# Kernel optimization log

Hardware: AMD Instinct MI355X
Metric: run time of the kernel (lower is better)

The kernel has to match this reference:

```python
import jax, jax.numpy as jnp
import numpy as np

N = 100000
E = 1600000
NUM_GRAPHS = 128
IN_C = 11
HID = 128


def setup_inputs() -> dict:
    key = jax.random.key(0)
    ks = jax.random.split(key, 16)
    x = jax.random.normal(ks[0], (N, IN_C), dtype=jnp.float32)
    edge_index = jax.random.randint(ks[1], (2, E), 0, N, dtype=jnp.int64)
    batch = jnp.sort(jax.random.randint(ks[2], (N,), 0, NUM_GRAPHS, dtype=jnp.int64))
    s_in = 1.0 / np.sqrt(IN_C)
    s_h = 1.0 / np.sqrt(HID)
    params = {
        'W1': jax.random.normal(ks[3], (IN_C, HID), jnp.float32) * s_in,
        'b1': jnp.zeros((HID,), jnp.float32),
        'W2': jax.random.normal(ks[4], (HID, HID), jnp.float32) * s_h,
        'b2': jnp.zeros((HID,), jnp.float32),
        'W4': jax.random.normal(ks[5], (HID, HID), jnp.float32) * s_h,
        'b4': jnp.zeros((HID,), jnp.float32),
        'Wd1': jax.random.normal(ks[6], (HID, HID), jnp.float32) * s_h,
        'bd1': jnp.zeros((HID,), jnp.float32),
        'Wd2': jax.random.normal(ks[7], (HID, HID), jnp.float32) * s_h,
        'bd2': jnp.zeros((HID,), jnp.float32),
        'Wo': jax.random.normal(ks[8], (HID, 1), jnp.float32) * s_h,
        'bo': jnp.zeros((1,), jnp.float32),
    }
    return {'x': x, 'edge_index': edge_index, 'batch': batch, **params}


def _gcn_norm(edge_index, n_nodes):
    # add self loops, compute symmetric normalization (PyG GCNConv defaults)
    loop = jnp.arange(n_nodes, dtype=edge_index.dtype)
    row = jnp.concatenate([edge_index[0], loop])
    col = jnp.concatenate([edge_index[1], loop])
    deg = jax.ops.segment_sum(jnp.ones_like(col, dtype=jnp.float32), col,
                              num_segments=n_nodes)
    dinv = jnp.where(deg > 0, jax.lax.rsqrt(deg), 0.0)
    norm = dinv[row] * dinv[col]  # [E+N]
    return row, col, norm


def _gcn_conv(h, row, col, norm, W, b, n_nodes):
    h = h @ W  # dense lin first (PyG order)
    msg = norm[:, None] * h[row]            # gather + normalize
    out = jax.ops.segment_sum(msg, col, num_segments=n_nodes)  # scatter-add
    return out + b


def reference(x, edge_index, batch, W1, b1, W2, b2, W4, b4,
              Wd1, bd1, Wd2, bd2, Wo, bo):
    n = x.shape[0]
    row, col, norm = _gcn_norm(edge_index, n)
    # dropout is identity in eval mode
    h = jax.nn.relu(_gcn_conv(x, row, col, norm, W1, b1, n))
    h = jax.nn.relu(_gcn_conv(h, row, col, norm, W2, b2, n))
    h = _gcn_conv(h, row, col, norm, W4, b4, n)
    # global_mean_pool over batch ids
    sums = jax.ops.segment_sum(h, batch, num_segments=NUM_GRAPHS)
    cnts = jax.ops.segment_sum(jnp.ones((n,), jnp.float32), batch,
                               num_segments=NUM_GRAPHS)
    g = sums / jnp.maximum(cnts, 1.0)[:, None]  # [NUM_GRAPHS, HID]
    g = jax.nn.relu(g @ Wd1 + bd1)
    g = jax.nn.relu(g @ Wd2 + bd2)
    return g @ Wo + bo  # [NUM_GRAPHS, 1]
```

## Files before the change

kernel.cpp:

```cpp
#include <hip/hip_runtime.h>
#include <hip/hip_fp16.h>

#define HIDDEN 128
#define BSHIFT 8
#define BMASK 255
#define CHUNK 4096
#define BCAP 6144

typedef _Float16 h8 __attribute__((ext_vector_type(8)));
typedef float f4x __attribute__((ext_vector_type(4)));

__global__ __launch_bounds__(256) void fill_bin(const int* __restrict__ row,
                                                const int* __restrict__ col,
                                                int* __restrict__ bcnt,
                                                int2* __restrict__ ptmp, int E) {
    __shared__ int cnt[512], start[512], place[512], gbase[512];
    __shared__ int ssum[256];
    __shared__ int2 stage[CHUNK];
    int t = threadIdx.x;
    int e0 = blockIdx.x * CHUNK;
    int e1 = min(e0 + CHUNK, E);
    cnt[t] = 0; cnt[t + 256] = 0;
    __syncthreads();
    for (int e = e0 + t; e < e1; e += 256)
        atomicAdd(&cnt[col[e] >> BSHIFT], 1);
    __syncthreads();
    int s2 = cnt[2 * t] + cnt[2 * t + 1];
    ssum[t] = s2;
    __syncthreads();
    for (int d = 1; d < 256; d <<= 1) {
        int v = (t >= d) ? ssum[t - d] : 0;
        __syncthreads();
        ssum[t] += v;
        __syncthreads();
    }
    int excl = ssum[t] - s2;
    start[2 * t] = excl;
    start[2 * t + 1] = excl + cnt[2 * t];
    place[2 * t] = excl;
    place[2 * t + 1] = excl + cnt[2 * t];
    __syncthreads();
    for (int e = e0 + t; e < e1; e += 256) {
        int c = col[e], r = row[e];
        int slot = atomicAdd(&place[c >> BSHIFT], 1);
        stage[slot] = make_int2(r, c);
    }
    {
        int c0 = cnt[t], c1 = cnt[t + 256];
        if (c0 > 0) gbase[t] = atomicAdd(&bcnt[t], c0);
        if (c1 > 0) gbase[t + 256] = atomicAdd(&bcnt[t + 256], c1);
    }
    __syncthreads();
    int n = e1 - e0;
    for (int i = t; i < n; i += 256) {
        int2 p = stage[i];
        int b = p.y >> BSHIFT;
        ptmp[(size_t)b * BCAP + gbase[b] + (i - start[b])] = p;
    }
}

__global__ __launch_bounds__(512) void scan_buckets(const int* __restrict__ bcnt,
                                                    int* __restrict__ bbase, int NB) {
    __shared__ int s[512];
    int t = threadIdx.x;
    int v0 = (t < NB) ? bcnt[t] : 0;
    s[t] = v0;
    __syncthreads();
    for (int d = 1; d < 512; d <<= 1) {
        int v = (t >= d) ? s[t - d] : 0;
        __syncthreads();
        s[t] += v;
        __syncthreads();
    }
    bbase[t] = s[t] - v0;
}

__global__ __launch_bounds__(256) void fill_scatter(const int2* __restrict__ ptmp,
                                                    const int* __restrict__ bcnt,
                                                    const int* __restrict__ bbase,
                                                    int* __restrict__ offsets,
                                                    float* __restrict__ dinv,
                                                    int* __restrict__ sorted_r,
                                                    int N, int E) {
    __shared__ int2 stage[BCAP];
    __shared__ int cnt[256], loff[256], cur[256];
    int b = blockIdx.x, t = threadIdx.x;
    int m = bcnt[b];
    int base = bbase[b];
    int nbase = b << BSHIFT;
    cnt[t] = 0;
    __syncthreads();
    for (int i = t; i < m; i += 256) {
        int2 p = ptmp[(size_t)b * BCAP + i];
        stage[i] = p;
        atomicAdd(&cnt[p.y & BMASK], 1);
    }
    __syncthreads();
    int my = cnt[t];
    loff[t] = my;
    __syncthreads();
    for (int d = 1; d < 256; d <<= 1) {
        int v = (t >= d) ? loff[t - d] : 0;
        __syncthreads();
        loff[t] += v;
        __syncthreads();
    }
    int excl = loff[t] - my;
    cur[t] = excl;
    int node = nbase + t;
    if (node < N) {
        offsets[node] = base + excl;
        dinv[node] = rsqrtf((float)(my + 1));
    }
    if (b == gridDim.x - 1 && t == 0) offsets[N] = E;
    __syncthreads();
    for (int i = t; i < m; i += 256) {
        int2 p = stage[i];
        int slot = atomicAdd(&cur[p.y & BMASK], 1);
        sorted_r[base + slot] = p.x;
    }
}

__global__ __launch_bounds__(256) void pad_x(const float* __restrict__ x,
                                             const float* __restrict__ dinv,
                                             __half* __restrict__ xp, int N) {
    int q = blockIdx.x * 256 + threadIdx.x;
    if (q >= N * 16) return;
    int i = q >> 4, c = q & 15;
    float v = (c < 11) ? x[(size_t)i * 11 + c] * dinv[i] : 0.f;
    xp[q] = __float2half(v);
}

__global__ __launch_bounds__(256) void agg16(const __half* __restrict__ xp,
                                             float* __restrict__ aggx,
                                             const int* __restrict__ offsets,
                                             const int* __restrict__ sorted_r,
                                             const float* __restrict__ dinv, int N) {
    int wid  = (blockIdx.x * 256 + threadIdx.x) >> 6;
    int lane = threadIdx.x & 63;
    if (wid >= N) return;
    int c = wid;
    int g = lane >> 3, cp = lane & 7;
    int beg = offsets[c], end = offsets[c + 1];
    const __half2* xp2 = (const __half2*)xp;
    float ax = 0.f, ay = 0.f;
    if (g == 0) {
        float2 v = __half22float2(xp2[(size_t)c * 8 + cp]);
        ax = v.x; ay = v.y;
    }
    for (int idx = beg + g; idx < end; idx += 8) {
        int r = sorted_r[idx];
        float2 v = __half22float2(xp2[(size_t)r * 8 + cp]);
        ax += v.x; ay += v.y;
    }
    ax += __shfl_xor(ax, 32); ay += __shfl_xor(ay, 32);
    ax += __shfl_xor(ax, 16); ay += __shfl_xor(ay, 16);
    ax += __shfl_xor(ax, 8);  ay += __shfl_xor(ay, 8);
    if (lane < 8) {
        float dc = dinv[c];
        aggx[(size_t)c * 16 + cp * 2]     = ax * dc;
        aggx[(size_t)c * 16 + cp * 2 + 1] = ay * dc;
    }
}

__global__ __launch_bounds__(256) void gemm_in_agg(const float* __restrict__ aggx,
                                                   const float* __restrict__ W1,
                                                   __half* __restrict__ out, int N) {
    int i = blockIdx.x * 2 + (threadIdx.x >> 7);
    int j = threadIdx.x & 127;
    if (i >= N) return;
    float acc = 0.f;
#pragma unroll
    for (int c = 0; c < 11; ++c) acc += aggx[(size_t)i * 16 + c] * W1[c * HIDDEN + j];
    out[(size_t)i * HIDDEN + j] = __float2half(acc);
}

__global__ __launch_bounds__(256) void pack_w(const float* __restrict__ W,
                                              const float* __restrict__ bias,
                                              __half* __restrict__ packed) {
    int q = blockIdx.x * 256 + threadIdx.x;
    if (q < 2048) {
        int s = q >> 9, rem = q & 511, ct = rem >> 6, l = rem & 63;
        int b = l >> 4, n = l & 15;
        __half hi8[8], lo8[8];
#pragma unroll
        for (int i = 0; i < 8; ++i) {
            float w = W[(s * 32 + b * 8 + i) * HIDDEN + ct * 16 + n];
            __half h = __float2half(w);
            hi8[i] = h;
            lo8[i] = __float2half(w - __half2float(h));
        }
        *(uint4*)(packed + (size_t)q * 8)         = *(uint4*)hi8;
        *(uint4*)(packed + 16384 + (size_t)q * 8) = *(uint4*)lo8;
    }
    if (q < 128) packed[32768 + q] = __float2half(bias[q]);
}

__global__ __launch_bounds__(256, 2) void gemm_mfma(const __half* __restrict__ H,
                                                    const __half* __restrict__ packed,
                                                    const float* __restrict__ dinv,
                                                    __half* __restrict__ out,
                                                    int N, int ngroups) {
    int l = threadIdx.x & 63, wv = threadIdx.x >> 6;
    int cthalf = wv & 1;
    int n16 = l & 15, koct = l >> 4;
    h8 whi[4][4], wlo[4][4];
#pragma unroll
    for (int s = 0; s < 4; ++s)
#pragma unroll
        for (int mt = 0; mt < 4; ++mt) {
            int ct = cthalf * 4 + mt;
            whi[s][mt] = *(const h8*)(packed + (size_t)((s * 8 + ct) * 64 + l) * 8);
            wlo[s][mt] = *(const h8*)(packed + 16384 + (size_t)((s * 8 + ct) * 64 + l) * 8);
        }
    h8 biasf[4];
    const __half* bias_h = packed + 32768;
#pragma unroll
    for (int s = 0; s < 4; ++s)
        biasf[s] = *(const h8*)(bias_h + s * 32 + koct * 8);

    for (int g = blockIdx.x * 2 + (wv >> 1); g < ngroups; g += gridDim.x * 2) {
        int node = g * 16 + n16;
        bool ok = node < N;
        f4x acc[4];
#pragma unroll
        for (int mt = 0; mt < 4; ++mt) acc[mt] = (f4x){0.f, 0.f, 0.f, 0.f};
#pragma unroll
        for (int s = 0; s < 4; ++s) {
            uint4 bv = make_uint4(0u, 0u, 0u, 0u);
            if (ok) bv = *(const uint4*)(H + (size_t)node * HIDDEN + s * 32 + koct * 8);
            __half2* bh2 = (__half2*)&bv;
            const __half2* bb = (const __half2*)&biasf[s];
#pragma unroll
            for (int p = 0; p < 4; ++p) {
                float2 f  = __half22float2(bh2[p]);
                float2 bf = __half22float2(bb[p]);
                bh2[p] = __floats2half2_rn(fmaxf(f.x + bf.x, 0.f), fmaxf(f.y + bf.y, 0.f));
            }
            h8 bfrag = *(h8*)&bv;
#pragma unroll
            for (int mt = 0; mt < 4; ++mt) {
                acc[mt] = __builtin_amdgcn_mfma_f32_16x16x32_f16(whi[s][mt], bfrag, acc[mt], 0, 0, 0);
                acc[mt] = __builtin_amdgcn_mfma_f32_16x16x32_f16(wlo[s][mt], bfrag, acc[mt], 0, 0, 0);
            }
        }
        if (ok) {
            float dv = dinv[node];
#pragma unroll
            for (int mt = 0; mt < 4; ++mt) {
                int ch = (cthalf * 4 + mt) * 16 + koct * 4;
                __half2 h01 = __floats2half2_rn(acc[mt][0] * dv, acc[mt][1] * dv);
                __half2 h23 = __floats2half2_rn(acc[mt][2] * dv, acc[mt][3] * dv);
                uint2 o;
                o.x = *(unsigned int*)&h01; o.y = *(unsigned int*)&h23;
                *(uint2*)(out + (size_t)node * HIDDEN + ch) = o;
            }
        }
    }
}

__global__ __launch_bounds__(256) void agg128h(const __half* __restrict__ src,
                                               __half* __restrict__ dst,
                                               const int* __restrict__ offsets,
                                               const int* __restrict__ sorted_r,
                                               const float* __restrict__ dinv, int N) {
    int wid  = (blockIdx.x * 256 + threadIdx.x) >> 6;
    int lane = threadIdx.x & 63;
    if (wid >= N) return;
    int c = wid;
    int beg = offsets[c], end = offsets[c + 1];
    int g = lane >> 4, sub = lane & 15;
    const uint4* hp = (const uint4*)src;
    float a0=0.f,a1=0.f,a2=0.f,a3=0.f,a4=0.f,a5=0.f,a6=0.f,a7=0.f;

    auto accum = [&](uint4 u) {
        __half2 p0 = *(__half2*)&u.x, p1 = *(__half2*)&u.y;
        __half2 p2 = *(__half2*)&u.z, p3 = *(__half2*)&u.w;
        float2 f0 = __half22float2(p0), f1 = __half22float2(p1);
        float2 f2 = __half22float2(p2), f3 = __half22float2(p3);
        a0 += f0.x; a1 += f0.y; a2 += f1.x; a3 += f1.y;
        a4 += f2.x; a5 += f2.y; a6 += f3.x; a7 += f3.y;
    };

    if (g == 0) accum(hp[(size_t)c * 16 + sub]);

    int i = beg;
    for (; i + 16 <= end; i += 16) {
        int base = i + 4 * g;
        int r0 = sorted_r[base + 0];
        int r1 = sorted_r[base + 1];
        int r2 = sorted_r[base + 2];
        int r3 = sorted_r[base + 3];
        uint4 u0 = hp[(size_t)r0 * 16 + sub];
        uint4 u1 = hp[(size_t)r1 * 16 + sub];
        uint4 u2 = hp[(size_t)r2 * 16 + sub];
        uint4 u3 = hp[(size_t)r3 * 16 + sub];
        accum(u0); accum(u1); accum(u2); accum(u3);
    }
    for (int idx = i + g; idx < end; idx += 4) {
        accum(hp[(size_t)sorted_r[idx] * 16 + sub]);
    }
    a0 += __shfl_xor(a0, 32); a1 += __shfl_xor(a1, 32);
    a2 += __shfl_xor(a2, 32); a3 += __shfl_xor(a3, 32);
    a4 += __shfl_xor(a4, 32); a5 += __shfl_xor(a5, 32);
    a6 += __shfl_xor(a6, 32); a7 += __shfl_xor(a7, 32);
    a0 += __shfl_xor(a0, 16); a1 += __shfl_xor(a1, 16);
    a2 += __shfl_xor(a2, 16); a3 += __shfl_xor(a3, 16);
    a4 += __shfl_xor(a4, 16); a5 += __shfl_xor(a5, 16);
    a6 += __shfl_xor(a6, 16); a7 += __shfl_xor(a7, 16);
    if (g == 0) {
        float dc = dinv[c];
        __half2 h01 = __floats2half2_rn(a0 * dc, a1 * dc);
        __half2 h23 = __floats2half2_rn(a2 * dc, a3 * dc);
        __half2 h45 = __floats2half2_rn(a4 * dc, a5 * dc);
        __half2 h67 = __floats2half2_rn(a6 * dc, a7 * dc);
        uint4 o;
        o.x = *(unsigned int*)&h01; o.y = *(unsigned int*)&h23;
        o.z = *(unsigned int*)&h45; o.w = *(unsigned int*)&h67;
        ((uint4*)dst)[(size_t)c * 16 + sub] = o;
    }
}

__global__ __launch_bounds__(256) void pool_partial(const __half* __restrict__ h,
                                                    const int* __restrict__ batch,
                                                    float* __restrict__ partials, int N) {
    int g = blockIdx.x >> 3, part8 = blockIdx.x & 7;
    int t = threadIdx.x, cp = t & 63, rp = t >> 6;
    int lo = 0, hi = N;
    while (lo < hi) { int m = (lo + hi) >> 1; if (batch[m] < g) lo = m + 1; else hi = m; }
    int beg = lo;
    lo = beg; hi = N;
    while (lo < hi) { int m = (lo + hi) >> 1; if (batch[m] < g + 1) lo = m + 1; else hi = m; }
    int end = lo;
    const __half2* h2 = (const __half2*)h;
    float ax = 0.f, ay = 0.f;
    for (int i = beg + part8 * 4 + rp; i < end; i += 32) {
        float2 v = __half22float2(h2[(size_t)i * 64 + cp]);
        ax += v.x; ay += v.y;
    }
    __shared__ float px[4][64], py[4][64];
    px[rp][cp] = ax; py[rp][cp] = ay;
    __syncthreads();
    if (rp == 0) {
        float sx = px[0][cp] + px[1][cp] + px[2][cp] + px[3][cp];
        float sy = py[0][cp] + py[1][cp] + py[2][cp] + py[3][cp];
        partials[(size_t)blockIdx.x * 128 + cp * 2]     = sx;
        partials[(size_t)blockIdx.x * 128 + cp * 2 + 1] = sy;
    }
}

__global__ __launch_bounds__(128) void head_kernel(const float* __restrict__ partials,
                                                   const int* __restrict__ batch,
                                                   const float* __restrict__ b4,
                                                   const float* __restrict__ Wd1,
                                                   const float* __restrict__ bd1,
                                                   const float* __restrict__ Wd2,
                                                   const float* __restrict__ bd2,
                                                   const float* __restrict__ Wo,
                                                   const float* __restrict__ bo,
                                                   float* __restrict__ out, int N) {
    int g = blockIdx.x;
    int j = threadIdx.x;
    __shared__ float sA[128], sB[128], red[128];
    int lo = 0, hi = N;
    while (lo < hi) { int m = (lo + hi) >> 1; if (batch[m] < g) lo = m + 1; else hi = m; }
    int beg = lo;
    lo = beg; hi = N;
    while (lo < hi) { int m = (lo + hi) >> 1; if (batch[m] < g + 1) lo = m + 1; else hi = m; }
    int cnt = lo - beg;
    float s = 0.f;
#pragma unroll
    for (int p = 0; p < 8; ++p) s += partials[(size_t)(g * 8 + p) * 128 + j];
    sA[j] = (cnt > 0) ? s / (float)cnt + b4[j] : 0.f;
    __syncthreads();
    float a = bd1[j];
#pragma unroll 4
    for (int k = 0; k < 128; ++k) a += sA[k] * Wd1[k * HIDDEN + j];
    sB[j] = fmaxf(a, 0.f);
    __syncthreads();
    a = bd2[j];
#pragma unroll 4
    for (int k = 0; k < 128; ++k) a += sB[k] * Wd2[k * HIDDEN + j];
    red[j] = fmaxf(a, 0.f) * Wo[j];
    __syncthreads();
    for (int d = 64; d > 0; d >>= 1) {
        if (j < d) red[j] += red[j + d];
        __syncthreads();
    }
    if (j == 0) out[g] = red[0] + bo[0];
}

extern "C" void kernel_launch(void* const* d_in, const int* in_sizes, int n_in,
                              void* d_out, int out_size, void* d_ws, size_t ws_size,
                              hipStream_t stream) {
    const float* x   = (const float*)d_in[0];
    const int*   ei  = (const int*)d_in[1];
    const int*   bat = (const int*)d_in[2];
    const float* W1  = (const float*)d_in[3];
    const float* b1  = (const float*)d_in[4];
    const float* W2  = (const float*)d_in[5];
    const float* b2  = (const float*)d_in[6];
    const float* W4  = (const float*)d_in[7];
    const float* b4  = (const float*)d_in[8];
    const float* Wd1 = (const float*)d_in[9];
    const float* bd1 = (const float*)d_in[10];
    const float* Wd2 = (const float*)d_in[11];
    const float* bd2 = (const float*)d_in[12];
    const float* Wo  = (const float*)d_in[13];
    const float* bo  = (const float*)d_in[14];
    float* out = (float*)d_out;

    const int N = in_sizes[0] / 11;
    const int E = in_sizes[1] / 2;
    const int* row = ei;
    const int* col = ei + E;
    const int B = (N + (1 << BSHIFT) - 1) >> BSHIFT;
    const int ngroups = (N + 15) / 16;

    size_t off = 0;
    auto carve = [&](size_t bytes) {
        void* p = (char*)d_ws + off;
        off += (bytes + 255) & ~(size_t)255;
        return p;
    };
    __half* bufHA    = (__half*)carve((size_t)N * HIDDEN * 2);
    __half* bufHB    = (__half*)carve((size_t)N * HIDDEN * 2);
    __half* xp       = (__half*)carve((size_t)N * 16 * 2);
    float*  aggx     = (float*)carve((size_t)N * 16 * 4);
    int*    offsets  = (int*)carve((size_t)(N + 1) * 4);
    float*  dinv     = (float*)carve((size_t)N * 4);
    int*    sorted_r = (int*)carve((size_t)E * 4);
    int*    bcnt     = (int*)carve((size_t)512 * 4);
    int*    bbase    = (int*)carve((size_t)512 * 4);
    float*  partials = (float*)carve((size_t)128 * 8 * 128 * 4);
    __half* packW2   = (__half*)carve((size_t)(32768 + 128) * 2);
    __half* packW4   = (__half*)carve((size_t)(32768 + 128) * 2);
    int2* ptmp = (int2*)bufHA;
    (void)ws_size; (void)n_in; (void)out_size;

    hipMemsetAsync(bcnt, 0, (size_t)512 * 4, stream);
    fill_bin<<<(E + CHUNK - 1) / CHUNK, 256, 0, stream>>>(row, col, bcnt, ptmp, E);
    scan_buckets<<<1, 512, 0, stream>>>(bcnt, bbase, B);
    fill_scatter<<<B, 256, 0, stream>>>(ptmp, bcnt, bbase, offsets, dinv,
                                        sorted_r, N, E);

    pack_w<<<8, 256, 0, stream>>>(W2, b1, packW2);
    pack_w<<<8, 256, 0, stream>>>(W4, b2, packW4);

    int aggBlocks = (N + 3) / 4;

    pad_x<<<(N * 16 + 255) / 256, 256, 0, stream>>>(x, dinv, xp, N);
    agg16<<<aggBlocks, 256, 0, stream>>>(xp, aggx, offsets, sorted_r, dinv, N);
    gemm_in_agg<<<(N + 1) / 2, 256, 0, stream>>>(aggx, W1, bufHA, N);
    gemm_mfma<<<1024, 256, 0, stream>>>(bufHA, packW2, dinv, bufHB, N, ngroups);
    agg128h<<<aggBlocks, 256, 0, stream>>>(bufHB, bufHA, offsets, sorted_r, dinv, N);
    gemm_mfma<<<1024, 256, 0, stream>>>(bufHA, packW4, dinv, bufHB, N, ngroups);
    agg128h<<<aggBlocks, 256, 0, stream>>>(bufHB, bufHA, offsets, sorted_r, dinv, N);
    pool_partial<<<128 * 8, 256, 0, stream>>>(bufHA, bat, partials, N);
    head_kernel<<<128, 128, 0, stream>>>(partials, bat, b4, Wd1, bd1, Wd2, bd2,
                                         Wo, bo, out, N);
}
```

Baseline: 333.6 us.

## Fuse x padding into fill_scatter and layer-1 aggregation with input GEMM

Computes the dinv-scaled, padded fp16 x rows inside fill_scatter, removing the separate pad_x launch. Merges the 16-wide neighbour aggregation with the 11x128 W1 product in one kernel that stages W1 and the aggregated rows in shared memory, so the fp32 aggx buffer is no longer written and re-read. It also unrolls the agg16 gather by two and replaces the tail loops in agg16 and agg128h with one clamped, predicated batch of loads. The cost is more shared-memory use, a block barrier in the fused kernel, and fill_scatter doing extra global loads and stores.

```diff
diff --git a/kernel.cpp b/kernel.cpp
--- a/kernel.cpp
+++ b/kernel.cpp
@@ -78,9 +78,11 @@
 __global__ __launch_bounds__(256) void fill_scatter(const int2* __restrict__ ptmp,
                                                     const int* __restrict__ bcnt,
                                                     const int* __restrict__ bbase,
+                                                    const float* __restrict__ x,
                                                     int* __restrict__ offsets,
                                                     float* __restrict__ dinv,
                                                     int* __restrict__ sorted_r,
+                                                    __half* __restrict__ xp,
                                                     int N, int E) {
     __shared__ int2 stage[BCAP];
     __shared__ int cnt[256], loff[256], cur[256];
@@ -108,9 +110,18 @@
     int excl = loff[t] - my;
     cur[t] = excl;
     int node = nbase + t;
+    float dv = rsqrtf((float)(my + 1));
     if (node < N) {
         offsets[node] = base + excl;
-        dinv[node] = rsqrtf((float)(my + 1));
+        dinv[node] = dv;
+        __half hrow[16];
+#pragma unroll
+        for (int c = 0; c < 11; ++c)
+            hrow[c] = __float2half(x[(size_t)node * 11 + c] * dv);
+#pragma unroll
+        for (int c = 11; c < 16; ++c) hrow[c] = __float2half(0.f);
+        *(uint4*)(xp + (size_t)node * 16)     = *(uint4*)hrow;
+        *(uint4*)(xp + (size_t)node * 16 + 8) = *(uint4*)(hrow + 8);
     }
     if (b == gridDim.x - 1 && t == 0) offsets[N] = E;
     __syncthreads();
@@ -121,58 +132,68 @@
     }
 }
 
-__global__ __launch_bounds__(256) void pad_x(const float* __restrict__ x,
-                                             const float* __restrict__ dinv,
-                                             __half* __restrict__ xp, int N) {
-    int q = blockIdx.x * 256 + threadIdx.x;
-    if (q >= N * 16) return;
-    int i = q >> 4, c = q & 15;
-    float v = (c < 11) ? x[(size_t)i * 11 + c] * dinv[i] : 0.f;
-    xp[q] = __float2half(v);
-}
-
-__global__ __launch_bounds__(256) void agg16(const __half* __restrict__ xp,
-                                             float* __restrict__ aggx,
-                                             const int* __restrict__ offsets,
-                                             const int* __restrict__ sorted_r,
-                                             const float* __restrict__ dinv, int N) {
-    int wid  = (blockIdx.x * 256 + threadIdx.x) >> 6;
-    int lane = threadIdx.x & 63;
-    if (wid >= N) return;
-    int c = wid;
+__global__ __launch_bounds__(256) void agg16_fused(const __half* __restrict__ xp,
+                                                   const float* __restrict__ W1,
+                                                   const int* __restrict__ offsets,
+                                                   const int* __restrict__ sorted_r,
+                                                   const float* __restrict__ dinv,
+                                                   __half* __restrict__ out, int N) {
+    __shared__ float W1s[11 * 128];
+    __shared__ float arow[4][16];
+    int t = threadIdx.x;
+    for (int q = t; q < 11 * 128; q += 256) W1s[q] = W1[q];
+    int wv = t >> 6, lane = t & 63;
+    int c = blockIdx.x * 4 + wv;
+    bool valid = c < N;
     int g = lane >> 3, cp = lane & 7;
-    int beg = offsets[c], end = offsets[c + 1];
     const __half2* xp2 = (const __half2*)xp;
     float ax = 0.f, ay = 0.f;
-    if (g == 0) {
-        float2 v = __half22float2(xp2[(size_t)c * 8 + cp]);
-        ax = v.x; ay = v.y;
-    }
-    for (int idx = beg + g; idx < end; idx += 8) {
-        int r = sorted_r[idx];
-        float2 v = __half22float2(xp2[(size_t)r * 8 + cp]);
-        ax += v.x; ay += v.y;
+    if (valid) {
+        int beg = offsets[c], end = offsets[c + 1];
+        if (g == 0) {
+            float2 v = __half22float2(xp2[(size_t)c * 8 + cp]);
+            ax = v.x; ay = v.y;
+        }
+        int i = beg;
+        for (; i + 16 <= end; i += 16) {
+            int r0 = sorted_r[i + g];
+            int r1 = sorted_r[i + g + 8];
+            float2 v0 = __half22float2(xp2[(size_t)r0 * 8 + cp]);
+            float2 v1 = __half22float2(xp2[(size_t)r1 * 8 + cp]);
+            ax += v0.x + v1.x; ay += v0.y + v1.y;
+        }
+        if (i < end) {
+            int last = end - 1;
+            int i0 = i + g, i1 = i + g + 8;
+            int r0 = sorted_r[min(i0, last)];
+            int r1 = sorted_r[min(i1, last)];
+            float2 v0 = __half22float2(xp2[(size_t)r0 * 8 + cp]);
+            float2 v1 = __half22float2(xp2[(size_t)r1 * 8 + cp]);
+            if (i0 <= last) { ax += v0.x; ay += v0.y; }
+            if (i1 <= last) { ax += v1.x; ay += v1.y; }
+        }
     }
     ax += __shfl_xor(ax, 32); ay += __shfl_xor(ay, 32);
     ax += __shfl_xor(ax, 16); ay += __shfl_xor(ay, 16);
     ax += __shfl_xor(ax, 8);  ay += __shfl_xor(ay, 8);
-    if (lane < 8) {
+    if (valid && lane < 8) {
         float dc = dinv[c];
-        aggx[(size_t)c * 16 + cp * 2]     = ax * dc;
-        aggx[(size_t)c * 16 + cp * 2 + 1] = ay * dc;
-    }
-}
-
-__global__ __launch_bounds__(256) void gemm_in_agg(const float* __restrict__ aggx,
-                                                   const float* __restrict__ W1,
-                                                   __half* __restrict__ out, int N) {
-    int i = blockIdx.x * 2 + (threadIdx.x >> 7);
-    int j = threadIdx.x & 127;
-    if (i >= N) return;
-    float acc = 0.f;
-#pragma unroll
-    for (int c = 0; c < 11; ++c) acc += aggx[(size_t)i * 16 + c] * W1[c * HIDDEN + j];
-    out[(size_t)i * HIDDEN + j] = __float2half(acc);
+        arow[wv][cp * 2]     = ax * dc;
+        arow[wv][cp * 2 + 1] = ay * dc;
+    }
+    __syncthreads();
+    int j = t & 127, half = t >> 7;
+#pragma unroll
+    for (int nn = 0; nn < 2; ++nn) {
+        int n = half * 2 + nn;
+        int node = blockIdx.x * 4 + n;
+        if (node < N) {
+            float acc = 0.f;
+#pragma unroll
+            for (int cc = 0; cc < 11; ++cc) acc += arow[n][cc] * W1s[cc * 128 + j];
+            out[(size_t)node * HIDDEN + j] = __float2half(acc);
+        }
+    }
 }
 
 __global__ __launch_bounds__(256) void pack_w(const float* __restrict__ W,
@@ -297,8 +318,21 @@
         uint4 u3 = hp[(size_t)r3 * 16 + sub];
         accum(u0); accum(u1); accum(u2); accum(u3);
     }
-    for (int idx = i + g; idx < end; idx += 4) {
-        accum(hp[(size_t)sorted_r[idx] * 16 + sub]);
+    if (i < end) {
+        int last = end - 1;
+        int i0 = i + 4 * g, i1 = i0 + 1, i2 = i0 + 2, i3 = i0 + 3;
+        int r0 = sorted_r[min(i0, last)];
+        int r1 = sorted_r[min(i1, last)];
+        int r2 = sorted_r[min(i2, last)];
+        int r3 = sorted_r[min(i3, last)];
+        uint4 u0 = hp[(size_t)r0 * 16 + sub];
+        uint4 u1 = hp[(size_t)r1 * 16 + sub];
+        uint4 u2 = hp[(size_t)r2 * 16 + sub];
+        uint4 u3 = hp[(size_t)r3 * 16 + sub];
+        if (i0 <= last) accum(u0);
+        if (i1 <= last) accum(u1);
+        if (i2 <= last) accum(u2);
+        if (i3 <= last) accum(u3);
     }
     a0 += __shfl_xor(a0, 32); a1 += __shfl_xor(a1, 32);
     a2 += __shfl_xor(a2, 32); a3 += __shfl_xor(a3, 32);
@@ -426,7 +460,6 @@
     __half* bufHA    = (__half*)carve((size_t)N * HIDDEN * 2);
     __half* bufHB    = (__half*)carve((size_t)N * HIDDEN * 2);
     __half* xp       = (__half*)carve((size_t)N * 16 * 2);
-    float*  aggx     = (float*)carve((size_t)N * 16 * 4);
     int*    offsets  = (int*)carve((size_t)(N + 1) * 4);
     float*  dinv     = (float*)carve((size_t)N * 4);
     int*    sorted_r = (int*)carve((size_t)E * 4);
@@ -441,17 +474,16 @@
     hipMemsetAsync(bcnt, 0, (size_t)512 * 4, stream);
     fill_bin<<<(E + CHUNK - 1) / CHUNK, 256, 0, stream>>>(row, col, bcnt, ptmp, E);
     scan_buckets<<<1, 512, 0, stream>>>(bcnt, bbase, B);
-    fill_scatter<<<B, 256, 0, stream>>>(ptmp, bcnt, bbase, offsets, dinv,
-                                        sorted_r, N, E);
+    fill_scatter<<<B, 256, 0, stream>>>(ptmp, bcnt, bbase, x, offsets, dinv,
+                                        sorted_r, xp, N, E);
 
     pack_w<<<8, 256, 0, stream>>>(W2, b1, packW2);
     pack_w<<<8, 256, 0, stream>>>(W4, b2, packW4);
 
     int aggBlocks = (N + 3) / 4;
 
-    pad_x<<<(N * 16 + 255) / 256, 256, 0, stream>>>(x, dinv, xp, N);
-    agg16<<<aggBlocks, 256, 0, stream>>>(xp, aggx, offsets, sorted_r, dinv, N);
-    gemm_in_agg<<<(N + 1) / 2, 256, 0, stream>>>(aggx, W1, bufHA, N);
+    agg16_fused<<<aggBlocks, 256, 0, stream>>>(xp, W1, offsets, sorted_r, dinv,
+                                               bufHA, N);
     gemm_mfma<<<1024, 256, 0, stream>>>(bufHA, packW2, dinv, bufHB, N, ngroups);
     agg128h<<<aggBlocks, 256, 0, stream>>>(bufHB, bufHA, offsets, sorted_r, dinv, N);
     gemm_mfma<<<1024, 256, 0, stream>>>(bufHA, packW4, dinv, bufHB, N, ngroups);
```

Result: faster. 310.4 us (-7.0%).
